# Kernel optimization log

Hardware: AMD Instinct MI355X
Metric: run time of the kernel (lower is better)

Reference implementation:

```python
import jax, jax.numpy as jnp
import numpy as np

N, E, IN_DIM, EDGE_DIM, EMB, H, L = 50000, 800000, 128, 32, 256, 8, 4
C = EMB // H  # per-head channels = 32
NEG_SLOPE = 0.2


def setup_inputs() -> dict:
    key = jax.random.key(0)
    ks = jax.random.split(key, 12)
    s = lambda d: 1.0 / np.sqrt(d)
    return {
        "x": jax.random.normal(ks[0], (N, IN_DIM), jnp.float32),
        "edge_index": jax.random.randint(ks[1], (2, E), 0, N, jnp.int32),
        "edge_attr": jax.random.normal(ks[2], (E, EDGE_DIM), jnp.float32),
        "w_in": jax.random.normal(ks[3], (IN_DIM, EMB), jnp.float32) * s(IN_DIM),
        "b_in": jnp.zeros((EMB,), jnp.float32),
        "W_l": jax.random.normal(ks[4], (L, EMB, EMB), jnp.float32) * s(EMB),
        "We_l": jax.random.normal(ks[5], (L, EDGE_DIM, EMB), jnp.float32) * s(EDGE_DIM),
        "att_src": jax.random.normal(ks[6], (L, H, C), jnp.float32) * s(C),
        "att_dst": jax.random.normal(ks[7], (L, H, C), jnp.float32) * s(C),
        "att_edge": jax.random.normal(ks[8], (L, H, C), jnp.float32) * s(C),
        "bias_l": jnp.zeros((L, EMB), jnp.float32),
        "w_out": jax.random.normal(ks[9], (EMB, 1), jnp.float32) * s(EMB),
        "b_out": jnp.zeros((1,), jnp.float32),
    }


def _gat_forward(x, edge_index, edge_attr, w_in, b_in, W_l, We_l,
                 att_src, att_dst, att_edge, bias_l, w_out, b_out):
    # add self loops (PyG GATConv default, edge_attr fill_value='mean')
    loop = jnp.arange(N, dtype=edge_index.dtype)
    src = jnp.concatenate([edge_index[0], loop])  # [E+N]
    dst = jnp.concatenate([edge_index[1], loop])
    ea = jnp.concatenate([edge_attr,
                          jnp.broadcast_to(edge_attr.mean(0), (N, EDGE_DIM))], 0)

    h = x @ w_in + b_in  # [N, EMB]
    for l in range(L):
        hp = (h @ W_l[l]).reshape(N, H, C)            # [N,H,C]
        ep = (ea @ We_l[l]).reshape(-1, H, C)         # [E+N,H,C]
        a_s = (hp * att_src[l]).sum(-1)               # [N,H]
        a_d = (hp * att_dst[l]).sum(-1)               # [N,H]
        e = a_s[src] + a_d[dst] + (ep * att_edge[l]).sum(-1)  # [E+N,H]
        e = jnp.where(e >= 0, e, NEG_SLOPE * e)
        # segment softmax over incoming edges of each dst node
        m = jax.ops.segment_max(e, dst, num_segments=N)
        e = jnp.exp(e - m[dst])
        denom = jax.ops.segment_sum(e, dst, num_segments=N)
        alpha = e / (denom[dst] + 1e-16)              # [E+N,H]
        msg = hp[src] * alpha[..., None]              # [E+N,H,C]
        h = jax.ops.segment_sum(msg, dst, num_segments=N).reshape(N, EMB) + bias_l[l]
    out = h @ w_out + b_out                           # [N,1]
    return out.squeeze(1)


def reference(x, edge_index, edge_attr, w_in, b_in, W_l, We_l,
              att_src, att_dst, att_edge, bias_l, w_out, b_out):
    return _gat_forward(x, edge_index, edge_attr, w_in, b_in, W_l, We_l,
                        att_src, att_dst, att_edge, bias_l, w_out, b_out)
```

## Files before the change

### kernel.cpp

```cpp
#include <hip/hip_runtime.h>

#define NN 50000
#define MPAD 50048
#define EE 800000
#define ETOT (EE + NN)
#define IN_DIM 128
#define EDGE_DIM 32
#define EMB 256
#define HH 8
#define LL 4
#define NEG_SLOPE 0.2f

typedef __attribute__((ext_vector_type(8))) short bf16x8;
typedef __attribute__((ext_vector_type(4))) float f32x4;

__device__ inline ushort f2bf_rn(float x) {
    union { float f; uint u; } v; v.f = x;
    uint r = v.u + 0x7FFFu + ((v.u >> 16) & 1u);
    return (ushort)(r >> 16);
}
__device__ inline float bf2f(ushort b) {
    union { uint u; float f; } v; v.u = ((uint)b) << 16;
    return v.f;
}

__device__ __forceinline__ void g2l16(const void* g, void* l) {
    __builtin_amdgcn_global_load_lds((const __attribute__((address_space(1))) void*)g,
                                     (__attribute__((address_space(3))) void*)l, 16, 0, 0);
}


__global__ void zero_int_kernel(int* p, int n) {
    int i = blockIdx.x * 256 + threadIdx.x;
    if (i < n) p[i] = 0;
}

__global__ void precompute_kernel(const float* __restrict__ We,
                                  const float* __restrict__ att_e,
                                  float* __restrict__ v) {
    int t = threadIdx.x;
    int l = t >> 8, rem = t & 255, d = rem >> 3, hh = rem & 7;
    float s = 0.f;
#pragma unroll
    for (int c = 0; c < 32; ++c)
        s += We[((size_t)(l * 32 + d)) * 256 + hh * 32 + c] * att_e[l * 256 + hh * 32 + c];
    v[t] = s;
}

__global__ __launch_bounds__(256) void col_partial(const float* __restrict__ ea,
                                                   float* __restrict__ part) {
    int t = threadIdx.x;
    int c = t & 7;
    int rg = t >> 3;
    float4 acc = {0.f, 0.f, 0.f, 0.f};
    for (int r = blockIdx.x * 32 + rg; r < EE; r += 1024 * 32) {
        float4 f = *(const float4*)&ea[(size_t)r * 32 + c * 4];
        acc.x += f.x; acc.y += f.y; acc.z += f.z; acc.w += f.w;
    }
    __shared__ float4 sm[256];
    sm[t] = acc;
    __syncthreads();
    for (int s = 16; s > 0; s >>= 1) {
        if (rg < s) {
            float4 o = sm[(rg + s) * 8 + c];
            float4 m = sm[t];
            m.x += o.x; m.y += o.y; m.z += o.z; m.w += o.w;
            sm[t] = m;
        }
        __syncthreads();
    }
    if (t < 8) *(float4*)&part[(size_t)blockIdx.x * 32 + t * 4] = sm[t];
}

__global__ __launch_bounds__(256) void col_final(const float* __restrict__ part,
                                                 float* __restrict__ mean_ea) {
    int t = threadIdx.x;
    int v = t & 31, c = t >> 5;
    float a0 = 0.f, a1 = 0.f, a2 = 0.f, a3 = 0.f;
    for (int b = c; b < 1024; b += 32) {
        a0 += part[(size_t)(b) * 32 + v];
        a1 += part[(size_t)(b + 8) * 32 + v];
        a2 += part[(size_t)(b + 16) * 32 + v];
        a3 += part[(size_t)(b + 24) * 32 + v];
    }
    float s = (a0 + a1) + (a2 + a3);
    __shared__ float sm[256];
    sm[t] = s;
    __syncthreads();
    if (c == 0) {
        float tot = 0.f;
#pragma unroll
        for (int k = 0; k < 8; ++k) tot += sm[k * 32 + v];
        mean_ea[v] = tot * (1.0f / EE);
    }
}

__global__ void hist_kernel(const int* __restrict__ ei, int* __restrict__ cnt) {
    int i = blockIdx.x * 256 + threadIdx.x;
    if (i >= ETOT) return;
    int dst = (i < EE) ? ei[EE + i] : (i - EE);
    atomicAdd(&cnt[dst], 1);
}

__global__ __launch_bounds__(256) void scan_phase1(const int* __restrict__ cnt,
                                                   int* __restrict__ bsum) {
    int b = blockIdx.x, t = threadIdx.x;
    int i0 = b * 1024 + t * 4;
    int s = 0;
#pragma unroll
    for (int r = 0; r < 4; ++r) s += (i0 + r < NN) ? cnt[i0 + r] : 0;
    for (int off = 1; off < 64; off <<= 1) s += __shfl_xor(s, off);
    __shared__ int wtot[4];
    if ((t & 63) == 0) wtot[t >> 6] = s;
    __syncthreads();
    if (t == 0) bsum[b] = wtot[0] + wtot[1] + wtot[2] + wtot[3];
}

__global__ void scan_phase2(int* __restrict__ bsum, int* __restrict__ row_ptr, int nb) {
    int lane = threadIdx.x;
    int vv = (lane < nb) ? bsum[lane] : 0;
    int incl = vv;
    for (int off = 1; off < 64; off <<= 1) {
        int u = __shfl_up(incl, off);
        if (lane >= off) incl += u;
    }
    if (lane < nb) bsum[lane] = incl - vv;
    if (lane == 0) row_ptr[NN] = ETOT;
}

__global__ __launch_bounds__(256) void scan_phase3(const int* __restrict__ cnt,
                                                   const int* __restrict__ bsum,
                                                   int* __restrict__ row_ptr,
                                                   int* __restrict__ fill) {
    int b = blockIdx.x, t = threadIdx.x;
    int i0 = b * 1024 + t * 4;
    int v[4];
    int s = 0;
#pragma unroll
    for (int r = 0; r < 4; ++r) { v[r] = (i0 + r < NN) ? cnt[i0 + r] : 0; s += v[r]; }
    int lane = t & 63, wv = t >> 6;
    int incl = s;
    for (int off = 1; off < 64; off <<= 1) {
        int u = __shfl_up(incl, off);
        if (lane >= off) incl += u;
    }
    __shared__ int wtot[4];
    if (lane == 63) wtot[wv] = incl;
    __syncthreads();
    int wpref = 0;
    for (int k = 0; k < wv; ++k) wpref += wtot[k];
    int start = bsum[b] + wpref + incl - s;
#pragma unroll
    for (int r = 0; r < 4; ++r) {
        int i = i0 + r;
        if (i < NN) { row_ptr[i] = start; fill[i] = start; }
        start += v[r];
    }
}

__global__ void scatter_kernel(const int* __restrict__ ei, int* __restrict__ fill,
                               int* __restrict__ sorted_src, int* __restrict__ sorted_eid) {
    int i = blockIdx.x * 256 + threadIdx.x;
    if (i >= ETOT) return;
    int dst, src;
    if (i < EE) { src = ei[i]; dst = ei[EE + i]; }
    else        { src = i - EE; dst = i - EE; }
    int pos = atomicAdd(&fill[dst], 1);
    sorted_src[pos] = src;
    sorted_eid[pos] = i;
}

__global__ __launch_bounds__(256) void split_weights(const float* __restrict__ w_in,
                                                     const float* __restrict__ W_l,
                                                     ushort* __restrict__ bh,
                                                     ushort* __restrict__ bl) {
    int t = blockIdx.x * 256 + threadIdx.x;
    if (t >= 32768 + 4 * 65536) return;
    float val;
    size_t dst;
    if (t < 32768) {
        int n = t >> 7, k = t & 127;
        val = w_in[(size_t)k * 256 + n];
        dst = (size_t)n * 128 + k;
    } else {
        int u = t - 32768;
        int l = u >> 16, r = u & 65535;
        int n = r >> 8, k = r & 255;
        val = W_l[(size_t)l * 65536 + (size_t)k * 256 + n];
        dst = 32768 + (size_t)l * 65536 + (size_t)n * 256 + k;
    }
    ushort hi = f2bf_rn(val);
    bh[dst] = hi;
    bl[dst] = f2bf_rn(val - bf2f(hi));
}

__global__ void split_x(const float* __restrict__ x, ushort* __restrict__ xh,
                        ushort* __restrict__ xl) {
    int i = blockIdx.x * 256 + threadIdx.x;
    if (i >= MPAD * 128) return;
    int n = i >> 7;
    float val = (n < NN) ? x[i] : 0.f;
    union { float f; uint u; } uv; uv.f = val;
    ushort hi = (ushort)(uv.u >> 16);
    xh[i] = hi;
    xl[i] = f2bf_rn(val - bf2f(hi));
}

__global__ __launch_bounds__(256) void edge_logits(const float* __restrict__ edge_attr,
                                                   const float* __restrict__ mean_ea,
                                                   const int* __restrict__ sorted_eid,
                                                   const float* __restrict__ v,
                                                   _Float16* __restrict__ e_all) {
    __shared__ float vs[1024];
    for (int t = threadIdx.x; t < 1024; t += 256) vs[t] = v[t];
    __syncthreads();
    int p = blockIdx.x * 256 + threadIdx.x;
    if (p >= ETOT) return;
    int eid = sorted_eid[p];
    const float4* row = (const float4*)((eid < EE) ? (edge_attr + (size_t)eid * 32) : mean_ea);
    float r[32];
#pragma unroll
    for (int q = 0; q < 8; ++q) {
        float4 f = row[q];
        r[q * 4] = f.x; r[q * 4 + 1] = f.y; r[q * 4 + 2] = f.z; r[q * 4 + 3] = f.w;
    }
    float acc[4][8] = {};
#pragma unroll 4
    for (int d = 0; d < 32; ++d) {
        float rv = r[d];
#pragma unroll
        for (int l = 0; l < 4; ++l)
#pragma unroll
            for (int h = 0; h < 8; ++h) acc[l][h] += rv * vs[l * 256 + d * 8 + h];
    }
#pragma unroll
    for (int l = 0; l < 4; ++l) {
        union { uint4 u; _Float16 h[8]; } pk;
#pragma unroll
        for (int h = 0; h < 8; ++h) pk.h[h] = (_Float16)acc[l][h];
        *(uint4*)&e_all[(size_t)l * ETOT * 8 + (size_t)p * 8] = pk.u;
    }
}

template <int MODE>
__global__ __launch_bounds__(256) void gemm_mfma(const ushort* __restrict__ Ah,
                                                 const ushort* __restrict__ Al,
                                                 const ushort* __restrict__ Bh,
                                                 const ushort* __restrict__ Bl,
                                                 const float* __restrict__ bias,
                                                 _Float16* __restrict__ hp_out,
                                                 ushort* __restrict__ hh_out,
                                                 ushort* __restrict__ hl_out,
                                                 int M, int K) {
    __shared__ __align__(16) ushort sAh[4096], sAl[4096], sBh[4096], sBl[4096];
    int tid = threadIdx.x;
    int m0 = blockIdx.x * 128, n0 = blockIdx.y * 128;
    int wid = tid >> 6, lane = tid & 63;
    int wm = wid & 1, wn = wid >> 1;
    int lr = lane & 15, grp = lane >> 4;
    f32x4 acc[4][4];
#pragma unroll
    for (int i = 0; i < 4; ++i)
#pragma unroll
        for (int j = 0; j < 4; ++j) acc[i][j] = (f32x4){0.f, 0.f, 0.f, 0.f};

    for (int k0 = 0; k0 < K; k0 += 32) {
        if (k0) __syncthreads();
#pragma unroll
        for (int i = 0; i < 2; ++i) {
            int ldso = wid * 1024 + i * 512;
            int o = ldso + lane * 8;
            int m = o >> 5;
            int cc = (o >> 3) & 3;
            int kl = ((cc ^ ((m >> 1) & 3)) << 3) + k0;
            size_t ga = (size_t)(m0 + m) * K + kl;
            size_t gb = (size_t)(n0 + m) * K + kl;
            g2l16(Ah + ga, sAh + ldso);
            g2l16(Al + ga, sAl + ldso);
            g2l16(Bh + gb, sBh + ldso);
            g2l16(Bl + gb, sBl + ldso);
        }
        __syncthreads();
        bf16x8 vbh[4], vbl[4];
#pragma unroll
        for (int j = 0; j < 4; ++j) {
            int n = wn * 64 + j * 16 + lr;
            int off = n * 32 + ((grp ^ ((n >> 1) & 3)) << 3);
            vbh[j] = *(const bf16x8*)&sBh[off];
            vbl[j] = *(const bf16x8*)&sBl[off];
        }
#pragma unroll
        for (int i = 0; i < 4; ++i) {
            int mm = wm * 64 + i * 16 + lr;
            int off = mm * 32 + ((grp ^ ((mm >> 1) & 3)) << 3);
            bf16x8 vah = *(const bf16x8*)&sAh[off];
            bf16x8 valo = *(const bf16x8*)&sAl[off];
#pragma unroll
            for (int j = 0; j < 4; ++j) {
                acc[i][j] = __builtin_amdgcn_mfma_f32_16x16x32_bf16(valo, vbh[j], acc[i][j], 0, 0, 0);
                acc[i][j] = __builtin_amdgcn_mfma_f32_16x16x32_bf16(vah, vbl[j], acc[i][j], 0, 0, 0);
                acc[i][j] = __builtin_amdgcn_mfma_f32_16x16x32_bf16(vah, vbh[j], acc[i][j], 0, 0, 0);
            }
        }
    }
#pragma unroll
    for (int j = 0; j < 4; ++j) {
        int c = n0 + wn * 64 + j * 16 + lr;
        float bj = (MODE == 0) ? bias[c] : 0.f;
#pragma unroll
        for (int i = 0; i < 4; ++i) {
            int mb = m0 + wm * 64 + i * 16 + grp * 4;
#pragma unroll
            for (int r = 0; r < 4; ++r) {
                int row = mb + r;
                if (row < M) {
                    float val = acc[i][j][r] + bj;
                    if (MODE == 0) {
                        union { float f; uint u; } uv; uv.f = val;
                        ushort hi = (ushort)(uv.u >> 16);
                        hh_out[(size_t)row * 256 + c] = hi;
                        hl_out[(size_t)row * 256 + c] = f2bf_rn(val - bf2f(hi));
                    } else {
                        hp_out[(size_t)row * 256 + c] = (_Float16)val;
                    }
                }
            }
        }
    }
}


__global__ __launch_bounds__(256) void a_sd_kernel(const _Float16* __restrict__ hp,
                                                   const float* __restrict__ att_s,
                                                   const float* __restrict__ att_d,
                                                   float* __restrict__ a_s,
                                                   float* __restrict__ a_d) {
    int idx = blockIdx.x * 256 + threadIdx.x;
    if (idx >= NN * 8) return;
    int n = idx >> 3, hh = idx & 7;
    const uint4* base = (const uint4*)(hp + (size_t)n * 256 + hh * 32);
    const float4* as4 = (const float4*)(att_s + hh * 32);
    const float4* ad4 = (const float4*)(att_d + hh * 32);
    float ss = 0.f, sd = 0.f;
#pragma unroll
    for (int q = 0; q < 4; ++q) {
        union { uint4 u; _Float16 f[8]; } hv;
        hv.u = base[q];
        float4 s0 = as4[q * 2], s1 = as4[q * 2 + 1];
        float4 d0 = ad4[q * 2], d1 = ad4[q * 2 + 1];
        float f0 = (float)hv.f[0], f1 = (float)hv.f[1], f2 = (float)hv.f[2], f3 = (float)hv.f[3];
        float f4 = (float)hv.f[4], f5 = (float)hv.f[5], f6 = (float)hv.f[6], f7 = (float)hv.f[7];
        ss += f0 * s0.x + f1 * s0.y + f2 * s0.z + f3 * s0.w + f4 * s1.x + f5 * s1.y + f6 * s1.z + f7 * s1.w;
        sd += f0 * d0.x + f1 * d0.y + f2 * d0.z + f3 * d0.w + f4 * d1.x + f5 * d1.y + f6 * d1.z + f7 * d1.w;
    }
    a_s[idx] = ss;
    a_d[idx] = sd;
}

__global__ __launch_bounds__(256) void aggregate_kernel(const _Float16* __restrict__ hp,
                                                        const float* __restrict__ a_s,
                                                        const float* __restrict__ a_d,
                                                        const _Float16* __restrict__ e_l,
                                                        const int* __restrict__ sorted_src,
                                                        const int* __restrict__ row_ptr,
                                                        const float* __restrict__ bias,
                                                        ushort* __restrict__ h_hi,
                                                        ushort* __restrict__ h_lo) {
    int n = (blockIdx.x * 256 + threadIdx.x) >> 6;
    if (n >= NN) return;
    int lane = threadIdx.x & 63;
    int h1 = lane & 7;
    int eslot = lane >> 3;
    int chan = lane & 31;
    int half = lane >> 5;
    int hh = chan >> 2;
    int beg = row_ptr[n], end = row_ptr[n + 1];
    float ad1 = a_d[n * 8 + h1];
    float s = 0.f;
    float acc[8] = {};

    int j0 = beg + eslot;
    bool valid = j0 < end;
    int jc = valid ? j0 : (end - 1);
    int srce = sorted_src[jc];
    float asv = a_s[srce * 8 + h1];
    float elv = (float)e_l[(size_t)jc * 8 + h1];

    for (int base = beg; base < end; base += 8) {
        int srce_n = 0; float asn = 0.f, eln = 0.f; bool nvalid = false;
        int nbase = base + 8;
        if (nbase < end) {
            int nj = nbase + eslot;
            nvalid = nj < end;
            int njc = nvalid ? nj : (end - 1);
            srce_n = sorted_src[njc];
            asn = a_s[srce_n * 8 + h1];
            eln = (float)e_l[(size_t)njc * 8 + h1];
        }
        float e = asv + ad1 + elv;
        e = (e >= 0.f) ? e : NEG_SLOPE * e;
        float w1 = valid ? __expf(e) : 0.f;
        float wv[4];
        int sv[4];
#pragma unroll
        for (int p = 0; p < 4; ++p) {
            int slot = p * 2 + half;
            wv[p] = __shfl(w1, slot * 8 + hh);
            sv[p] = __shfl(srce, slot * 8);
        }
        union { uint4 u; _Float16 q[8]; } hv[4];
#pragma unroll
        for (int p = 0; p < 4; ++p)
            hv[p].u = *(const uint4*)&hp[(size_t)sv[p] * 256 + chan * 8];
#pragma unroll
        for (int p = 0; p < 4; ++p) {
            float w = wv[p];
            s += w;
#pragma unroll
            for (int k = 0; k < 8; ++k) acc[k] += w * (float)hv[p].q[k];
        }
        srce = srce_n; asv = asn; elv = eln; valid = nvalid;
    }
    s += __shfl_xor(s, 32);
#pragma unroll
    for (int k = 0; k < 8; ++k) acc[k] += __shfl_xor(acc[k], 32);

    float inv = 1.0f / (s + 1e-16f);
    const float4* b4 = (const float4*)&bias[chan * 8];
    float4 bA = b4[0], bB = b4[1];
    float o[8];
    o[0] = acc[0] * inv + bA.x; o[1] = acc[1] * inv + bA.y;
    o[2] = acc[2] * inv + bA.z; o[3] = acc[3] * inv + bA.w;
    o[4] = acc[4] * inv + bB.x; o[5] = acc[5] * inv + bB.y;
    o[6] = acc[6] * inv + bB.z; o[7] = acc[7] * inv + bB.w;
    union { uint4 u; ushort v[8]; } pk;
    if (half == 0) {
#pragma unroll
        for (int k = 0; k < 8; ++k) {
            union { float f; uint u; } uv; uv.f = o[k];
            pk.v[k] = (ushort)(uv.u >> 16);
        }
        *(uint4*)&h_hi[(size_t)n * 256 + chan * 8] = pk.u;
    } else {
#pragma unroll
        for (int k = 0; k < 8; ++k) {
            union { float f; uint u; } uv; uv.f = o[k];
            ushort hi = (ushort)(uv.u >> 16);
            pk.v[k] = f2bf_rn(o[k] - bf2f(hi));
        }
        *(uint4*)&h_lo[(size_t)n * 256 + chan * 8] = pk.u;
    }
}

__global__ __launch_bounds__(256) void out_kernel(const ushort* __restrict__ h_hi,
                                                  const ushort* __restrict__ h_lo,
                                                  const float* __restrict__ w_out,
                                                  const float* __restrict__ b_out,
                                                  float* __restrict__ out) {
    int n = (blockIdx.x * 256 + threadIdx.x) >> 6;
    if (n >= NN) return;
    int lane = threadIdx.x & 63;
    union { uint2 u; ushort s[4]; } uh, ul;
    uh.u = *(const uint2*)&h_hi[(size_t)n * 256 + lane * 4];
    ul.u = *(const uint2*)&h_lo[(size_t)n * 256 + lane * 4];
    const float4 wv = *(const float4*)&w_out[lane * 4];
    float s = (bf2f(uh.s[0]) + bf2f(ul.s[0])) * wv.x +
              (bf2f(uh.s[1]) + bf2f(ul.s[1])) * wv.y +
              (bf2f(uh.s[2]) + bf2f(ul.s[2])) * wv.z +
              (bf2f(uh.s[3]) + bf2f(ul.s[3])) * wv.w;
    for (int off = 1; off < 64; off <<= 1) s += __shfl_xor(s, off);
    if (lane == 0) out[n] = s + b_out[0];
}


extern "C" void kernel_launch(void* const* d_in, const int* in_sizes, int n_in,
                              void* d_out, int out_size, void* d_ws, size_t ws_size,
                              hipStream_t stream) {
    const float* x         = (const float*)d_in[0];
    const int*   edge_idx  = (const int*)d_in[1];
    const float* edge_attr = (const float*)d_in[2];
    const float* w_in      = (const float*)d_in[3];
    const float* b_in      = (const float*)d_in[4];
    const float* W_l       = (const float*)d_in[5];
    const float* We_l      = (const float*)d_in[6];
    const float* att_src   = (const float*)d_in[7];
    const float* att_dst   = (const float*)d_in[8];
    const float* att_edge  = (const float*)d_in[9];
    const float* bias_l    = (const float*)d_in[10];
    const float* w_out     = (const float*)d_in[11];
    const float* b_out     = (const float*)d_in[12];
    float* out = (float*)d_out;

    char* ws = (char*)d_ws;
    size_t off = 0;
    auto alloc = [&](size_t bytes) -> void* {
        void* p = ws + off;
        off = (off + bytes + 255) & ~(size_t)255;
        return p;
    };
    ushort*   h_hi       = (ushort*)alloc((size_t)MPAD * 256 * 2);
    ushort*   h_lo       = (ushort*)alloc((size_t)MPAD * 256 * 2);
    _Float16* hp16       = (_Float16*)alloc((size_t)MPAD * 256 * 2);
    float*    a_s        = (float*)alloc((size_t)NN * 8 * 4);
    float*    a_d        = (float*)alloc((size_t)NN * 8 * 4);
    int*      sorted_src = (int*)alloc((size_t)ETOT * 4);
    int*      sorted_eid = (int*)alloc((size_t)ETOT * 4);
    int*      row_ptr    = (int*)alloc((size_t)(NN + 1) * 4);
    int*      fill       = (int*)alloc((size_t)NN * 4);
    int*      cnt        = (int*)alloc((size_t)NN * 4);
    int*      bsum       = (int*)alloc(64 * 4);
    float*    col_part   = (float*)alloc((size_t)1024 * 32 * 4);
    float*    mean_ea    = (float*)alloc(32 * 4);
    float*    v          = (float*)alloc(1024 * 4);
    ushort*   bsp_hi     = (ushort*)alloc((size_t)294912 * 2);
    ushort*   bsp_lo     = (ushort*)alloc((size_t)294912 * 2);
    char*     uni        = (char*)alloc((size_t)4 * ETOT * 8 * 2);
    ushort*   xh         = (ushort*)uni;
    ushort*   xl         = (ushort*)(uni + (size_t)MPAD * 128 * 2);
    _Float16* e_all      = (_Float16*)uni;

    const int NB = (NN + 1023) / 1024;

    zero_int_kernel<<<(NN + 255) / 256, 256, 0, stream>>>(cnt, NN);
    precompute_kernel<<<1, 1024, 0, stream>>>(We_l, att_edge, v);
    col_partial<<<1024, 256, 0, stream>>>(edge_attr, col_part);
    col_final<<<1, 256, 0, stream>>>(col_part, mean_ea);
    split_weights<<<(294912 + 255) / 256, 256, 0, stream>>>(w_in, W_l, bsp_hi, bsp_lo);
    split_x<<<(MPAD * 128 + 255) / 256, 256, 0, stream>>>(x, xh, xl);

    dim3 ggrid((NN + 127) / 128, 2);
    gemm_mfma<0><<<ggrid, 256, 0, stream>>>(xh, xl, bsp_hi, bsp_lo, b_in,
                                            nullptr, h_hi, h_lo, NN, IN_DIM);

    hist_kernel<<<(ETOT + 255) / 256, 256, 0, stream>>>(edge_idx, cnt);
    scan_phase1<<<NB, 256, 0, stream>>>(cnt, bsum);
    scan_phase2<<<1, 64, 0, stream>>>(bsum, row_ptr, NB);
    scan_phase3<<<NB, 256, 0, stream>>>(cnt, bsum, row_ptr, fill);
    scatter_kernel<<<(ETOT + 255) / 256, 256, 0, stream>>>(edge_idx, fill, sorted_src, sorted_eid);
    edge_logits<<<(ETOT + 255) / 256, 256, 0, stream>>>(edge_attr, mean_ea, sorted_eid, v, e_all);

    for (int l = 0; l < LL; ++l) {
        const ushort* wh = bsp_hi + 32768 + (size_t)l * 65536;
        const ushort* wl = bsp_lo + 32768 + (size_t)l * 65536;
        gemm_mfma<1><<<ggrid, 256, 0, stream>>>(h_hi, h_lo, wh, wl, nullptr,
                                                hp16, nullptr, nullptr, NN, EMB);
        a_sd_kernel<<<(NN * 8 + 255) / 256, 256, 0, stream>>>(
            hp16, att_src + l * 256, att_dst + l * 256, a_s, a_d);
        aggregate_kernel<<<NN / 4, 256, 0, stream>>>(
            hp16, a_s, a_d, e_all + (size_t)l * ETOT * 8, sorted_src, row_ptr,
            bias_l + l * 256, h_hi, h_lo);
    }

    out_kernel<<<NN / 4, 256, 0, stream>>>(h_hi, h_lo, w_out, b_out, out);
}
```

Before: 739.8 us.

## Double GEMM K-tile to 64 and fuse output projection into last aggregation

The MFMA GEMM now stages 64-wide K slices instead of 32, with a new XOR swizzle over 8 column groups. This halves the number of barrier and load rounds per tile, at the cost of doubling LDS use to 64KB per block, which may reduce occupancy. Separately, the final aggregate layer computes the dot product with w_out directly. That removes the out_kernel launch and the last write and read of h_hi and h_lo.

```diff
diff --git a/kernel.cpp b/kernel.cpp
--- a/kernel.cpp
+++ b/kernel.cpp
@@ -252,7 +252,7 @@
                                                  ushort* __restrict__ hh_out,
                                                  ushort* __restrict__ hl_out,
                                                  int M, int K) {
-    __shared__ __align__(16) ushort sAh[4096], sAl[4096], sBh[4096], sBl[4096];
+    __shared__ __align__(16) ushort sAh[8192], sAl[8192], sBh[8192], sBl[8192];
     int tid = threadIdx.x;
     int m0 = blockIdx.x * 128, n0 = blockIdx.y * 128;
     int wid = tid >> 6, lane = tid & 63;
@@ -264,15 +264,14 @@
 #pragma unroll
         for (int j = 0; j < 4; ++j) acc[i][j] = (f32x4){0.f, 0.f, 0.f, 0.f};
 
-    for (int k0 = 0; k0 < K; k0 += 32) {
+    for (int k0 = 0; k0 < K; k0 += 64) {
         if (k0) __syncthreads();
 #pragma unroll
-        for (int i = 0; i < 2; ++i) {
-            int ldso = wid * 1024 + i * 512;
+        for (int i = 0; i < 4; ++i) {
+            int ldso = wid * 2048 + i * 512;
             int o = ldso + lane * 8;
-            int m = o >> 5;
-            int cc = (o >> 3) & 3;
-            int kl = ((cc ^ ((m >> 1) & 3)) << 3) + k0;
+            int m = o >> 6;
+            int kl = ((((o >> 3) & 7) ^ (m & 7)) << 3) + k0;
             size_t ga = (size_t)(m0 + m) * K + kl;
             size_t gb = (size_t)(n0 + m) * K + kl;
             g2l16(Ah + ga, sAh + ldso);
@@ -281,25 +280,28 @@
             g2l16(Bl + gb, sBl + ldso);
         }
         __syncthreads();
-        bf16x8 vbh[4], vbl[4];
-#pragma unroll
-        for (int j = 0; j < 4; ++j) {
-            int n = wn * 64 + j * 16 + lr;
-            int off = n * 32 + ((grp ^ ((n >> 1) & 3)) << 3);
-            vbh[j] = *(const bf16x8*)&sBh[off];
-            vbl[j] = *(const bf16x8*)&sBl[off];
-        }
-#pragma unroll
-        for (int i = 0; i < 4; ++i) {
-            int mm = wm * 64 + i * 16 + lr;
-            int off = mm * 32 + ((grp ^ ((mm >> 1) & 3)) << 3);
-            bf16x8 vah = *(const bf16x8*)&sAh[off];
-            bf16x8 valo = *(const bf16x8*)&sAl[off];
+#pragma unroll
+        for (int ks = 0; ks < 2; ++ks) {
+            bf16x8 vbh[4], vbl[4];
 #pragma unroll
             for (int j = 0; j < 4; ++j) {
-                acc[i][j] = __builtin_amdgcn_mfma_f32_16x16x32_bf16(valo, vbh[j], acc[i][j], 0, 0, 0);
-                acc[i][j] = __builtin_amdgcn_mfma_f32_16x16x32_bf16(vah, vbl[j], acc[i][j], 0, 0, 0);
-                acc[i][j] = __builtin_amdgcn_mfma_f32_16x16x32_bf16(vah, vbh[j], acc[i][j], 0, 0, 0);
+                int n = wn * 64 + j * 16 + lr;
+                int off = n * 64 + ((ks * 32 + grp * 8) ^ ((n & 7) << 3));
+                vbh[j] = *(const bf16x8*)&sBh[off];
+                vbl[j] = *(const bf16x8*)&sBl[off];
+            }
+#pragma unroll
+            for (int i = 0; i < 4; ++i) {
+                int mm = wm * 64 + i * 16 + lr;
+                int off = mm * 64 + ((ks * 32 + grp * 8) ^ ((mm & 7) << 3));
+                bf16x8 vah = *(const bf16x8*)&sAh[off];
+                bf16x8 valo = *(const bf16x8*)&sAl[off];
+#pragma unroll
+                for (int j = 0; j < 4; ++j) {
+                    acc[i][j] = __builtin_amdgcn_mfma_f32_16x16x32_bf16(valo, vbh[j], acc[i][j], 0, 0, 0);
+                    acc[i][j] = __builtin_amdgcn_mfma_f32_16x16x32_bf16(vah, vbl[j], acc[i][j], 0, 0, 0);
+                    acc[i][j] = __builtin_amdgcn_mfma_f32_16x16x32_bf16(vah, vbh[j], acc[i][j], 0, 0, 0);
+                }
             }
         }
     }
@@ -357,6 +359,7 @@
     a_d[idx] = sd;
 }
 
+template <int LAST>
 __global__ __launch_bounds__(256) void aggregate_kernel(const _Float16* __restrict__ hp,
                                                         const float* __restrict__ a_s,
                                                         const float* __restrict__ a_d,
@@ -365,7 +368,10 @@
                                                         const int* __restrict__ row_ptr,
                                                         const float* __restrict__ bias,
                                                         ushort* __restrict__ h_hi,
-                                                        ushort* __restrict__ h_lo) {
+                                                        ushort* __restrict__ h_lo,
+                                                        const float* __restrict__ w_out,
+                                                        const float* __restrict__ b_out,
+                                                        float* __restrict__ out) {
     int n = (blockIdx.x * 256 + threadIdx.x) >> 6;
     if (n >= NN) return;
     int lane = threadIdx.x & 63;
@@ -433,6 +439,15 @@
     o[2] = acc[2] * inv + bA.z; o[3] = acc[3] * inv + bA.w;
     o[4] = acc[4] * inv + bB.x; o[5] = acc[5] * inv + bB.y;
     o[6] = acc[6] * inv + bB.z; o[7] = acc[7] * inv + bB.w;
+    if (LAST) {
+        const float4* w4 = (const float4*)&w_out[chan * 8];
+        float4 wA = w4[0], wB = w4[1];
+        float dot = o[0] * wA.x + o[1] * wA.y + o[2] * wA.z + o[3] * wA.w +
+                    o[4] * wB.x + o[5] * wB.y + o[6] * wB.z + o[7] * wB.w;
+        for (int off = 1; off < 32; off <<= 1) dot += __shfl_xor(dot, off);
+        if (lane == 0) out[n] = dot + b_out[0];
+        return;
+    }
     union { uint4 u; ushort v[8]; } pk;
     if (half == 0) {
 #pragma unroll
@@ -450,26 +465,6 @@
         }
         *(uint4*)&h_lo[(size_t)n * 256 + chan * 8] = pk.u;
     }
-}
-
-__global__ __launch_bounds__(256) void out_kernel(const ushort* __restrict__ h_hi,
-                                                  const ushort* __restrict__ h_lo,
-                                                  const float* __restrict__ w_out,
-                                                  const float* __restrict__ b_out,
-                                                  float* __restrict__ out) {
-    int n = (blockIdx.x * 256 + threadIdx.x) >> 6;
-    if (n >= NN) return;
-    int lane = threadIdx.x & 63;
-    union { uint2 u; ushort s[4]; } uh, ul;
-    uh.u = *(const uint2*)&h_hi[(size_t)n * 256 + lane * 4];
-    ul.u = *(const uint2*)&h_lo[(size_t)n * 256 + lane * 4];
-    const float4 wv = *(const float4*)&w_out[lane * 4];
-    float s = (bf2f(uh.s[0]) + bf2f(ul.s[0])) * wv.x +
-              (bf2f(uh.s[1]) + bf2f(ul.s[1])) * wv.y +
-              (bf2f(uh.s[2]) + bf2f(ul.s[2])) * wv.z +
-              (bf2f(uh.s[3]) + bf2f(ul.s[3])) * wv.w;
-    for (int off = 1; off < 64; off <<= 1) s += __shfl_xor(s, off);
-    if (lane == 0) out[n] = s + b_out[0];
 }
 
 
@@ -546,10 +541,14 @@
                                                 hp16, nullptr, nullptr, NN, EMB);
         a_sd_kernel<<<(NN * 8 + 255) / 256, 256, 0, stream>>>(
             hp16, att_src + l * 256, att_dst + l * 256, a_s, a_d);
-        aggregate_kernel<<<NN / 4, 256, 0, stream>>>(
-            hp16, a_s, a_d, e_all + (size_t)l * ETOT * 8, sorted_src, row_ptr,
-            bias_l + l * 256, h_hi, h_lo);
-    }
-
-    out_kernel<<<NN / 4, 256, 0, stream>>>(h_hi, h_lo, w_out, b_out, out);
-}
+        if (l < LL - 1) {
+            aggregate_kernel<0><<<NN / 4, 256, 0, stream>>>(
+                hp16, a_s, a_d, e_all + (size_t)l * ETOT * 8, sorted_src, row_ptr,
+                bias_l + l * 256, h_hi, h_lo, nullptr, nullptr, nullptr);
+        } else {
+            aggregate_kernel<1><<<NN / 4, 256, 0, stream>>>(
+                hp16, a_s, a_d, e_all + (size_t)l * ETOT * 8, sorted_src, row_ptr,
+                bias_l + l * 256, nullptr, nullptr, w_out, b_out, out);
+        }
+    }
+}
```

Result: faster. 696.3 us (-5.9%).
